# Performance work log

Measured on AMD Instinct MI355X. Metric: run time of the kernel, lower is better.

Reference implementation:

```python
import jax, jax.numpy as jnp
import numpy as np

C = 512       # num_features
M = 8192      # num_quantities
EPS = 1e-12   # F.normalize default eps


def _l2norm(x, axis):
    n = jnp.sqrt(jnp.sum(x * x, axis=axis, keepdims=True))
    return x / jnp.maximum(n, EPS)


def setup_inputs() -> dict:
    key = jax.random.key(0)
    k1, k2 = jax.random.split(key)
    x = jax.random.normal(k1, (8, 4096, C), dtype=jnp.float32)
    embeddings = jax.random.normal(k2, (C, M), dtype=jnp.float32)
    return {"x": x, "embeddings": embeddings}


def reference(x, embeddings):
    ellip_shape = x.shape[:-1]
    flat = x.reshape(-1, x.shape[-1])                 # [N, C]
    flat = _l2norm(flat, axis=-1)                     # row-normalize tokens
    norm_emb = _l2norm(embeddings, axis=0)            # [C, M], column-normalize codebook
    sims = jnp.einsum('nc,cm->nm', flat, norm_emb)    # [N, M] cosine similarities
    best = jnp.argmax(sims, axis=1)                   # [N]
    # F.embedding(idx, norm_emb.T): gather codebook columns as rows
    quantized = jnp.take(norm_emb.T, best, axis=0)    # [N, C]
    return quantized.reshape(*ellip_shape, x.shape[-1])
```

## Files before the change

### kernel.cpp

```cpp
#include <hip/hip_runtime.h>
#include <hip/hip_bf16.h>
#include <stdint.h>
#include <math.h>

#define C_DIM 512
#define M_DIM 8192
#define N_TOK 32768
#define MSPLIT 8
#define MARGIN 8e-3f

typedef _Float16 f16;
typedef _Float16 f16x8 __attribute__((ext_vector_type(8)));
typedef float f32x4 __attribute__((ext_vector_type(4)));

__global__ void k_colnorm(const float* __restrict__ emb, float* __restrict__ inv,
                          double* __restrict__ inv64) {
    int m = blockIdx.x * 256 + threadIdx.x;
    double s = 0.0;
    for (int c = 0; c < C_DIM; ++c) {
        double v = (double)emb[(size_t)c * M_DIM + m];
        s += v * v;
    }
    double r = 1.0 / fmax(sqrt(s), 1e-12);
    inv[m] = (float)r;
    inv64[m] = r;
}

__global__ void k_xprep(const float* __restrict__ x, f16* __restrict__ xh) {
    int i = (blockIdx.x * 256 + threadIdx.x) * 8;
    float4 a = *(const float4*)&x[i];
    float4 b = *(const float4*)&x[i + 4];
    f16x8 h;
    h[0] = (f16)a.x; h[1] = (f16)a.y; h[2] = (f16)a.z; h[3] = (f16)a.w;
    h[4] = (f16)b.x; h[5] = (f16)b.y; h[6] = (f16)b.z; h[7] = (f16)b.w;
    *(f16x8*)&xh[i] = h;
}

__global__ void k_eprep(const float* __restrict__ emb, const float* __restrict__ inv,
                        f16* __restrict__ eTh, float* __restrict__ normT) {
    __shared__ float t[32][33];
    int m0 = blockIdx.x * 32, k0 = blockIdx.y * 32;
    int tx = threadIdx.x, ty = threadIdx.y;
    for (int r = ty; r < 32; r += 8)
        t[r][tx] = emb[(size_t)(k0 + r) * M_DIM + m0 + tx];
    __syncthreads();
    for (int r = ty; r < 32; r += 8) {
        float v = t[tx][r];
        int m = m0 + r;
        eTh[(size_t)m * C_DIM + k0 + tx] = (f16)v;
        normT[(size_t)m * C_DIM + k0 + tx] = v * inv[m];
    }
}

__launch_bounds__(256, 2)
__global__ void k_gemm(const f16* __restrict__ xh, const f16* __restrict__ eTh,
                       const float* __restrict__ inv,
                       float* __restrict__ pv1, int* __restrict__ pi1,
                       float* __restrict__ pv2) {
    __shared__ __align__(16) f16 xs[128 * 32];
    __shared__ __align__(16) f16 es[128 * 32];
    const int tid = threadIdx.x;
    const int lane = tid & 63, wid = tid >> 6;
    const int n0 = blockIdx.x * 128;
    const int by = blockIdx.y;
    const int l15 = lane & 15, l4 = lane >> 4;
    const f32x4 ZERO = {0.f, 0.f, 0.f, 0.f};

    float v1[8], v2[8]; int i1[8];
#pragma unroll
    for (int r = 0; r < 8; ++r) { v1[r] = -1e30f; v2[r] = -1e30f; i1[r] = 0; }

    for (int mt = 0; mt < 8; ++mt) {
        const int mbase = by * 1024 + mt * 128;
        f32x4 acc[2][8];
#pragma unroll
        for (int a = 0; a < 2; ++a)
#pragma unroll
            for (int b = 0; b < 8; ++b) acc[a][b] = ZERO;

        for (int kt = 0; kt < 16; ++kt) {
            __syncthreads();
            {
                int L = tid;
#pragma unroll
                for (int it = 0; it < 2; ++it, L += 256) {
                    int row = L >> 2, ch = (L & 3) * 8;
                    *(f16x8*)&xs[row * 32 + ch] =
                        *(const f16x8*)&xh[(size_t)(n0 + row) * C_DIM + kt * 32 + ch];
                    *(f16x8*)&es[row * 32 + ch] =
                        *(const f16x8*)&eTh[(size_t)(mbase + row) * C_DIM + kt * 32 + ch];
                }
            }
            __syncthreads();
            f16x8 A[2];
#pragma unroll
            for (int fr = 0; fr < 2; ++fr)
                A[fr] = *(const f16x8*)&xs[(wid * 32 + fr * 16 + l15) * 32 + l4 * 8];
#pragma unroll
            for (int fc = 0; fc < 8; ++fc) {
                f16x8 B = *(const f16x8*)&es[(fc * 16 + l15) * 32 + l4 * 8];
#pragma unroll
                for (int fr = 0; fr < 2; ++fr)
                    acc[fr][fc] = __builtin_amdgcn_mfma_f32_16x16x32_f16(A[fr], B, acc[fr][fc], 0, 0, 0);
            }
        }
#pragma unroll
        for (int fc = 0; fc < 8; ++fc) {
            int m = mbase + fc * 16 + l15;
            float iv = inv[m];
#pragma unroll
            for (int fr = 0; fr < 2; ++fr) {
#pragma unroll
                for (int j = 0; j < 4; ++j) {
                    float v = acc[fr][fc][j] * iv;
                    int slot = fr * 4 + j;
                    if (v > v1[slot]) { v2[slot] = v1[slot]; v1[slot] = v; i1[slot] = m; }
                    else if (v > v2[slot]) { v2[slot] = v; }
                }
            }
        }
    }

#pragma unroll
    for (int slot = 0; slot < 8; ++slot) {
        int fr = slot >> 2, j = slot & 3;
        float v = v1[slot], w = v2[slot]; int ix = i1[slot];
#pragma unroll
        for (int off = 1; off < 16; off <<= 1) {
            float ov = __shfl_xor(v, off);
            int  oix = __shfl_xor(ix, off);
            float ow = __shfl_xor(w, off);
            bool owin = (ov > v) || (ov == v && oix < ix);
            if (owin) { w = fmaxf(v, ow); v = ov; ix = oix; }
            else      { w = fmaxf(w, ov); }
        }
        if (l15 == 0) {
            int n = n0 + wid * 32 + fr * 16 + l4 * 4 + j;
            pv1[(size_t)by * N_TOK + n] = v;
            pi1[(size_t)by * N_TOK + n] = ix;
            pv2[(size_t)by * N_TOK + n] = w;
        }
    }
}

__global__ void k_merge_flag(const float* __restrict__ pv1, const int* __restrict__ pi1,
                             const float* __restrict__ pv2,
                             int* __restrict__ best, int* __restrict__ list,
                             int* __restrict__ count) {
    int n = blockIdx.x * 256 + threadIdx.x;
    float v = pv1[n]; int ix = pi1[n]; float w = pv2[n];
    for (int s = 1; s < MSPLIT; ++s) {
        float ov = pv1[(size_t)s * N_TOK + n];
        int  oix = pi1[(size_t)s * N_TOK + n];
        float ow = pv2[(size_t)s * N_TOK + n];
        bool owin = (ov > v) || (ov == v && oix < ix);
        if (owin) { w = fmaxf(v, ow); v = ov; ix = oix; }
        else      { w = fmaxf(w, ov); }
    }
    best[n] = ix;
    if (v - w < MARGIN) {
        int p = atomicAdd(count, 1);
        list[p] = n;
    }
}

#define RROWS 16
template <bool IDENT>
__global__ void k_rescan(const float* __restrict__ x, const float* __restrict__ emb,
                         const double* __restrict__ inv64, const int* __restrict__ list,
                         const int* __restrict__ countp,
                         double* __restrict__ prv, int* __restrict__ pri) {
    __shared__ __align__(16) float xsh[RROWS * C_DIM];
    __shared__ double wred_v[4][RROWS];
    __shared__ int    wred_i[4][RROWS];
    const int tid = threadIdx.x, lane = tid & 63, wid = tid >> 6;
    const int by = blockIdx.y;
    const int cnt = IDENT ? N_TOK : *countp;
    const int ntiles = (cnt + RROWS - 1) / RROWS;

    for (int tile = blockIdx.x; tile < ntiles; tile += gridDim.x) {
        __syncthreads();
        for (int it = 0; it < 8; ++it) {
            int lin = tid + it * 256;
            int row = lin >> 7, c4 = (lin & 127) << 2;
            int p = tile * RROWS + row;
            float4 val = make_float4(0.f, 0.f, 0.f, 0.f);
            if (p < cnt) {
                int n = IDENT ? p : list[p];
                val = *(const float4*)&x[(size_t)n * C_DIM + c4];
            }
            *(float4*)&xsh[row * C_DIM + c4] = val;
        }
        __syncthreads();

        double bv[RROWS]; int bi[RROWS];
#pragma unroll
        for (int i = 0; i < RROWS; ++i) { bv[i] = -1e300; bi[i] = 0; }

        for (int jj = 0; jj < 4; ++jj) {
            const int m = by * 1024 + jj * 256 + tid;
            double acc[RROWS];
#pragma unroll
            for (int i = 0; i < RROWS; ++i) acc[i] = 0.0;
            for (int c = 0; c < C_DIM; c += 4) {
                double b0 = (double)emb[(size_t)(c + 0) * M_DIM + m];
                double b1 = (double)emb[(size_t)(c + 1) * M_DIM + m];
                double b2 = (double)emb[(size_t)(c + 2) * M_DIM + m];
                double b3 = (double)emb[(size_t)(c + 3) * M_DIM + m];
#pragma unroll
                for (int i = 0; i < RROWS; ++i) {
                    float4 a = *(const float4*)&xsh[i * C_DIM + c];
                    acc[i] = fma((double)a.x, b0, fma((double)a.y, b1,
                              fma((double)a.z, b2, fma((double)a.w, b3, acc[i]))));
                }
            }
            double iv = inv64[m];
#pragma unroll
            for (int i = 0; i < RROWS; ++i) {
                double v = acc[i] * iv;
                if (v > bv[i]) { bv[i] = v; bi[i] = m; }
            }
        }
#pragma unroll
        for (int i = 0; i < RROWS; ++i) {
            double v = bv[i]; int ix = bi[i];
#pragma unroll
            for (int off = 1; off < 64; off <<= 1) {
                double ov = __shfl_xor(v, off);
                int   oix = __shfl_xor(ix, off);
                if (ov > v || (ov == v && oix < ix)) { v = ov; ix = oix; }
            }
            if (lane == 0) { wred_v[wid][i] = v; wred_i[wid][i] = ix; }
        }
        __syncthreads();
        if (tid < RROWS) {
            int i = tid;
            double v = wred_v[0][i]; int ix = wred_i[0][i];
            for (int wdx = 1; wdx < 4; ++wdx) {
                double ov = wred_v[wdx][i]; int oix = wred_i[wdx][i];
                if (ov > v || (ov == v && oix < ix)) { v = ov; ix = oix; }
            }
            int p = tile * RROWS + i;
            if (p < cnt) {
                prv[(size_t)by * N_TOK + p] = v;
                pri[(size_t)by * N_TOK + p] = ix;
            }
        }
    }
}

template <bool IDENT>
__global__ void k_merge2(const double* __restrict__ prv, const int* __restrict__ pri,
                         const int* __restrict__ list, const int* __restrict__ countp,
                         int* __restrict__ best) {
    int p = blockIdx.x * 256 + threadIdx.x;
    const int cnt = IDENT ? N_TOK : *countp;
    if (p >= cnt) return;
    double v = prv[p]; int ix = pri[p];
    for (int s = 1; s < MSPLIT; ++s) {
        double ov = prv[(size_t)s * N_TOK + p];
        int   oix = pri[(size_t)s * N_TOK + p];
        if (ov > v || (ov == v && oix < ix)) { v = ov; ix = oix; }
    }
    best[IDENT ? p : list[p]] = ix;
}

__global__ void k_gather(const float* __restrict__ normT, const int* __restrict__ best,
                         float* __restrict__ out) {
    int n = blockIdx.x;
    int b = best[n];
    int c = threadIdx.x * 4;
    *(float4*)&out[(size_t)n * C_DIM + c] = *(const float4*)&normT[(size_t)b * C_DIM + c];
}

__global__ void k_gather_fb(const float* __restrict__ emb, const float* __restrict__ inv,
                            const int* __restrict__ best, float* __restrict__ out) {
    int n = blockIdx.x;
    int b = best[n];
    float iv = inv[b];
    for (int c = threadIdx.x; c < C_DIM; c += 128)
        out[(size_t)n * C_DIM + c] = emb[(size_t)c * M_DIM + b] * iv;
}

extern "C" void kernel_launch(void* const* d_in, const int* in_sizes, int n_in,
                              void* d_out, int out_size, void* d_ws, size_t ws_size,
                              hipStream_t stream) {
    const float* x   = (const float*)d_in[0];
    const float* emb = (const float*)d_in[1];
    float* out = (float*)d_out;
    char* ws = (char*)d_ws;

    float*  inv   = (float*) (ws + 0);
    double* inv64 = (double*)(ws + 32768);
    f16*    xh    = (f16*)   (ws + 98304);
    f16*    eTh   = (f16*)   (ws + 33652736);
    float*  normT = (float*) (ws + 42041344);
    float*  pv1   = (float*) (ws + 58818560);
    int*    pi1   = (int*)   (ws + 59867136);
    float*  pv2   = (float*) (ws + 60915712);
    int*    best  = (int*)   (ws + 61964288);
    int*    list  = (int*)   (ws + 62095360);
    int*    count = (int*)   (ws + 62226432);
    double* prv   = (double*)(ws + 62226688);
    int*    pri   = (int*)   (ws + 64323840);
    const size_t NEED = 65372416;

    if (ws_size >= NEED) {
        hipMemsetAsync(count, 0, 4, stream);
        k_colnorm<<<M_DIM / 256, 256, 0, stream>>>(emb, inv, inv64);
        k_xprep<<<(N_TOK * C_DIM) / (256 * 8), 256, 0, stream>>>(x, xh);
        k_eprep<<<dim3(M_DIM / 32, C_DIM / 32), dim3(32, 8), 0, stream>>>(emb, inv, eTh, normT);
        k_gemm<<<dim3(N_TOK / 128, MSPLIT), 256, 0, stream>>>(xh, eTh, inv, pv1, pi1, pv2);
        k_merge_flag<<<N_TOK / 256, 256, 0, stream>>>(pv1, pi1, pv2, best, list, count);
        k_rescan<false><<<dim3(64, MSPLIT), 256, 0, stream>>>(x, emb, inv64, list, count, prv, pri);
        k_merge2<false><<<N_TOK / 256, 256, 0, stream>>>(prv, pri, list, count, best);
        k_gather<<<N_TOK, 128, 0, stream>>>(normT, best, out);
    } else {
        float*  f_inv   = (float*) (ws + 0);
        double* f_inv64 = (double*)(ws + 32768);
        double* f_prv   = (double*)(ws + 98304);
        int*    f_pri   = (int*)   (ws + 2195456);
        int*    f_best  = (int*)   (ws + 3244032);
        k_colnorm<<<M_DIM / 256, 256, 0, stream>>>(emb, f_inv, f_inv64);
        k_rescan<true><<<dim3(256, MSPLIT), 256, 0, stream>>>(x, emb, f_inv64, nullptr, nullptr, f_prv, f_pri);
        k_merge2<true><<<N_TOK / 256, 256, 0, stream>>>(f_prv, f_pri, nullptr, nullptr, f_best);
        k_gather_fb<<<N_TOK, 128, 0, stream>>>(emb, f_inv, f_best, out);
    }
}
```

Baseline: 1.094 ms.

## Load GEMM tiles directly into LDS with swizzled layout and tighter margin

Replaces register-staged global-to-LDS copies in the similarity GEMM with direct global_load_lds 16-byte transfers. An XOR swizzle on row slots is applied both when writing and when reading, to avoid LDS bank conflicts on the MFMA fragment loads. Precomputes per-thread source and LDS offsets outside the loops. Also lowers the refinement margin from 8e-3 to 5e-3, which may send fewer tokens to the exact re-check but risks wrong argmax picks if fp16 error exceeds the margin.

Result: no change. 1.075 ms (-1.7%).

```diff
diff --git a/kernel.cpp b/kernel.cpp
--- a/kernel.cpp
+++ b/kernel.cpp
@@ -7,11 +7,18 @@
 #define M_DIM 8192
 #define N_TOK 32768
 #define MSPLIT 8
-#define MARGIN 8e-3f
+#define MARGIN 5e-3f
 
 typedef _Float16 f16;
 typedef _Float16 f16x8 __attribute__((ext_vector_type(8)));
 typedef float f32x4 __attribute__((ext_vector_type(4)));
+
+typedef const __attribute__((address_space(1))) void gas_void;
+typedef __attribute__((address_space(3))) void las_void;
+
+__device__ __forceinline__ void gl16(const void* g, void* l) {
+    __builtin_amdgcn_global_load_lds((gas_void*)g, (las_void*)l, 16, 0, 0);
+}
 
 __global__ void k_colnorm(const float* __restrict__ emb, float* __restrict__ inv,
                           double* __restrict__ inv64) {
@@ -66,12 +73,37 @@
     const int l15 = lane & 15, l4 = lane >> 4;
     const f32x4 ZERO = {0.f, 0.f, 0.f, 0.f};
 
+    const int row0 = tid >> 2,        slot0 = (tid & 3) ^ ((tid >> 3) & 3);
+    const int row1 = (tid + 256) >> 2, slot1 = (tid & 3) ^ (((tid + 256) >> 3) & 3);
+    const int so0 = row0 * C_DIM + slot0 * 8;
+    const int so1 = row1 * C_DIM + slot1 * 8;
+    char* xsb = (char*)xs; char* esb = (char*)es;
+    char* xd0 = xsb + wid * 1024; char* xd1 = xsb + 4096 + wid * 1024;
+    char* ed0 = esb + wid * 1024; char* ed1 = esb + 4096 + wid * 1024;
+
+    int aoff[2], boff[8];
+#pragma unroll
+    for (int fr = 0; fr < 2; ++fr) {
+        int r = wid * 32 + fr * 16 + l15;
+        aoff[fr] = (r * 64 + l4 * 16) ^ (((r >> 1) & 3) << 4);
+    }
+#pragma unroll
+    for (int fc = 0; fc < 8; ++fc) {
+        int r = fc * 16 + l15;
+        boff[fc] = (r * 64 + l4 * 16) ^ (((r >> 1) & 3) << 4);
+    }
+
+    const f16* xp0 = xh + (size_t)n0 * C_DIM + so0;
+    const f16* xp1 = xh + (size_t)n0 * C_DIM + so1;
+
     float v1[8], v2[8]; int i1[8];
 #pragma unroll
     for (int r = 0; r < 8; ++r) { v1[r] = -1e30f; v2[r] = -1e30f; i1[r] = 0; }
 
     for (int mt = 0; mt < 8; ++mt) {
         const int mbase = by * 1024 + mt * 128;
+        const f16* ep0 = eTh + (size_t)mbase * C_DIM + so0;
+        const f16* ep1 = eTh + (size_t)mbase * C_DIM + so1;
         f32x4 acc[2][8];
 #pragma unroll
         for (int a = 0; a < 2; ++a)
@@ -80,25 +112,18 @@
 
         for (int kt = 0; kt < 16; ++kt) {
             __syncthreads();
-            {
-                int L = tid;
-#pragma unroll
-                for (int it = 0; it < 2; ++it, L += 256) {
-                    int row = L >> 2, ch = (L & 3) * 8;
-                    *(f16x8*)&xs[row * 32 + ch] =
-                        *(const f16x8*)&xh[(size_t)(n0 + row) * C_DIM + kt * 32 + ch];
-                    *(f16x8*)&es[row * 32 + ch] =
-                        *(const f16x8*)&eTh[(size_t)(mbase + row) * C_DIM + kt * 32 + ch];
-                }
-            }
+            gl16(xp0 + kt * 32, xd0);
+            gl16(xp1 + kt * 32, xd1);
+            gl16(ep0 + kt * 32, ed0);
+            gl16(ep1 + kt * 32, ed1);
             __syncthreads();
             f16x8 A[2];
 #pragma unroll
             for (int fr = 0; fr < 2; ++fr)
-                A[fr] = *(const f16x8*)&xs[(wid * 32 + fr * 16 + l15) * 32 + l4 * 8];
+                A[fr] = *(const f16x8*)(xsb + aoff[fr]);
 #pragma unroll
             for (int fc = 0; fc < 8; ++fc) {
-                f16x8 B = *(const f16x8*)&es[(fc * 16 + l15) * 32 + l4 * 8];
+                f16x8 B = *(const f16x8*)(esb + boff[fc]);
 #pragma unroll
                 for (int fr = 0; fr < 2; ++fr)
                     acc[fr][fc] = __builtin_amdgcn_mfma_f32_16x16x32_f16(A[fr], B, acc[fr][fc], 0, 0, 0);
```

## Double-buffer GEMM tiles via direct global-to-LDS loads with XOR swizzle

Applied to the files above, without the earlier changes.

Rewrites the k_gemm main loop to stage 64-wide K tiles directly from global memory into LDS using global_load_lds, double-buffered so the next tile loads while MFMAs run on the current one. It adds an XOR swizzle on the LDS layout to avoid bank conflicts, halves the number of K iterations and barriers, and prefetches the next M-tile's first chunk across the tile boundary. It also tightens the fp16 rescoring margin, which lets fewer candidate tokens fall back to exact recheck but increases the risk of wrong argmax near ties. LDS use grows to 64KB per block, which may limit occupancy.

Result: slower. 1.132 ms (+3.5%).

```diff
diff --git a/kernel.cpp b/kernel.cpp
--- a/kernel.cpp
+++ b/kernel.cpp
@@ -7,11 +7,18 @@
 #define M_DIM 8192
 #define N_TOK 32768
 #define MSPLIT 8
-#define MARGIN 8e-3f
+#define MARGIN 3e-3f
 
 typedef _Float16 f16;
 typedef _Float16 f16x8 __attribute__((ext_vector_type(8)));
 typedef float f32x4 __attribute__((ext_vector_type(4)));
+
+typedef const __attribute__((address_space(1))) void gas_void;
+typedef __attribute__((address_space(3))) void las_void;
+
+__device__ __forceinline__ void gl16(const void* g, void* l) {
+    __builtin_amdgcn_global_load_lds((gas_void*)g, (las_void*)l, 16, 0, 0);
+}
 
 __global__ void k_colnorm(const float* __restrict__ emb, float* __restrict__ inv,
                           double* __restrict__ inv64) {
@@ -52,13 +59,19 @@
     }
 }
 
+#define STAGE(XO, EO, BB) do {                                              \
+    _Pragma("unroll")                                                       \
+    for (int c = 0; c < 4; ++c) {                                           \
+        gl16(xptr[c] + (XO), lds + (BB) + c * 4096 + wid * 1024);           \
+        gl16(eptr[c] + (EO), lds + 32768 + (BB) + c * 4096 + wid * 1024);   \
+    } } while (0)
+
 __launch_bounds__(256, 2)
 __global__ void k_gemm(const f16* __restrict__ xh, const f16* __restrict__ eTh,
                        const float* __restrict__ inv,
                        float* __restrict__ pv1, int* __restrict__ pi1,
                        float* __restrict__ pv2) {
-    __shared__ __align__(16) f16 xs[128 * 32];
-    __shared__ __align__(16) f16 es[128 * 32];
+    __shared__ __align__(16) char lds[65536];
     const int tid = threadIdx.x;
     const int lane = tid & 63, wid = tid >> 6;
     const int n0 = blockIdx.x * 128;
@@ -66,9 +79,34 @@
     const int l15 = lane & 15, l4 = lane >> 4;
     const f32x4 ZERO = {0.f, 0.f, 0.f, 0.f};
 
+    int soff[4];
+#pragma unroll
+    for (int c = 0; c < 4; ++c) {
+        int L = c * 256 + tid;
+        int row = L >> 3;
+        int slot = (L & 7) ^ (row & 7);
+        soff[c] = row * C_DIM + slot * 8;
+    }
+    const f16* xptr[4]; const f16* eptr[4];
+#pragma unroll
+    for (int c = 0; c < 4; ++c) {
+        xptr[c] = xh + (size_t)n0 * C_DIM + soff[c];
+        eptr[c] = eTh + (size_t)by * 1024 * C_DIM + soff[c];
+    }
+    const int sw = (l15 & 7) << 4;
+    const int q0 = (l4 * 16) ^ sw;
+    const int q1 = (64 + l4 * 16) ^ sw;
+    const int pA0 = (wid * 32 + l15) * 128 + q0;
+    const int pA1 = (wid * 32 + l15) * 128 + q1;
+    const int pB0 = l15 * 128 + q0;
+    const int pB1 = l15 * 128 + q1;
+
     float v1[8], v2[8]; int i1[8];
 #pragma unroll
     for (int r = 0; r < 8; ++r) { v1[r] = -1e30f; v2[r] = -1e30f; i1[r] = 0; }
+
+    STAGE(0, 0, 0);
+    __syncthreads();
 
     for (int mt = 0; mt < 8; ++mt) {
         const int mbase = by * 1024 + mt * 128;
@@ -78,31 +116,31 @@
 #pragma unroll
             for (int b = 0; b < 8; ++b) acc[a][b] = ZERO;
 
-        for (int kt = 0; kt < 16; ++kt) {
-            __syncthreads();
-            {
-                int L = tid;
-#pragma unroll
-                for (int it = 0; it < 2; ++it, L += 256) {
-                    int row = L >> 2, ch = (L & 3) * 8;
-                    *(f16x8*)&xs[row * 32 + ch] =
-                        *(const f16x8*)&xh[(size_t)(n0 + row) * C_DIM + kt * 32 + ch];
-                    *(f16x8*)&es[row * 32 + ch] =
-                        *(const f16x8*)&eTh[(size_t)(mbase + row) * C_DIM + kt * 32 + ch];
+#pragma unroll
+        for (int kt = 0; kt < 8; ++kt) {
+            const int cur = kt & 1;
+            if (kt < 7) {
+                if (cur == 0) STAGE((kt + 1) * 64, (kt + 1) * 64, 16384);
+                else          STAGE((kt + 1) * 64, (kt + 1) * 64, 0);
+            } else if (mt < 7) {
+                STAGE(0, 128 * C_DIM, 0);
+            }
+            const int xb = cur * 16384;
+            const int eb = 32768 + cur * 16384;
+#pragma unroll
+            for (int kk = 0; kk < 2; ++kk) {
+                const int qA = kk ? pA1 : pA0;
+                const int qB = kk ? pB1 : pB0;
+                f16x8 A0 = *(const f16x8*)(lds + xb + qA);
+                f16x8 A1 = *(const f16x8*)(lds + xb + qA + 2048);
+#pragma unroll
+                for (int fc = 0; fc < 8; ++fc) {
+                    f16x8 B = *(const f16x8*)(lds + eb + qB + fc * 2048);
+                    acc[0][fc] = __builtin_amdgcn_mfma_f32_16x16x32_f16(A0, B, acc[0][fc], 0, 0, 0);
+                    acc[1][fc] = __builtin_amdgcn_mfma_f32_16x16x32_f16(A1, B, acc[1][fc], 0, 0, 0);
                 }
             }
-            __syncthreads();
-            f16x8 A[2];
-#pragma unroll
-            for (int fr = 0; fr < 2; ++fr)
-                A[fr] = *(const f16x8*)&xs[(wid * 32 + fr * 16 + l15) * 32 + l4 * 8];
-#pragma unroll
-            for (int fc = 0; fc < 8; ++fc) {
-                f16x8 B = *(const f16x8*)&es[(fc * 16 + l15) * 32 + l4 * 8];
-#pragma unroll
-                for (int fr = 0; fr < 2; ++fr)
-                    acc[fr][fc] = __builtin_amdgcn_mfma_f32_16x16x32_f16(A[fr], B, acc[fr][fc], 0, 0, 0);
-            }
+            if (kt < 7) __syncthreads();
         }
 #pragma unroll
         for (int fc = 0; fc < 8; ++fc) {
@@ -119,6 +157,9 @@
                 }
             }
         }
+        __syncthreads();
+#pragma unroll
+        for (int c = 0; c < 4; ++c) eptr[c] += 128 * C_DIM;
     }
 
 #pragma unroll
```
